# Optimization experiments

Measured on AMD Instinct MI355X. Metric: run time of the kernel, lower is better.

Reference implementation:

```python
import jax, jax.numpy as jnp
import numpy as np

N_NODES = 50000
N_EDGES = 800000
IN_FEATS = 128
HEADS = 4
OUT_FEATS = 32
NEG_SLOPE = 0.2


def setup_inputs() -> dict:
    key = jax.random.key(0)
    ks = jax.random.split(key, 9)
    HD = HEADS * OUT_FEATS
    return {
        "feat": jax.random.normal(ks[0], (N_NODES, IN_FEATS), dtype=jnp.float32),
        "W_src": jax.random.normal(ks[1], (HD, IN_FEATS), dtype=jnp.float32) * (1.0 / np.sqrt(IN_FEATS)),
        "b_src": jax.random.normal(ks[2], (HD,), dtype=jnp.float32) * 0.02,
        "W_dst": jax.random.normal(ks[3], (HD, IN_FEATS), dtype=jnp.float32) * (1.0 / np.sqrt(IN_FEATS)),
        "b_dst": jax.random.normal(ks[4], (HD,), dtype=jnp.float32) * 0.02,
        "W_v": jax.random.normal(ks[5], (HD, IN_FEATS), dtype=jnp.float32) * (1.0 / np.sqrt(IN_FEATS)),
        "b_v": jax.random.normal(ks[6], (HD,), dtype=jnp.float32) * 0.02,
        "src": jax.random.randint(ks[7], (N_EDGES,), 0, N_NODES, dtype=jnp.int32),
        "dst": jax.random.randint(ks[8], (N_EDGES,), 0, N_NODES, dtype=jnp.int32),
    }


def _edge_softmax(e, dst, n_nodes):
    # segment softmax over incoming edges of each dst node; e: [E, H, D]
    seg_max = jax.ops.segment_max(e, dst, num_segments=n_nodes)  # [N, H, D]
    ex = jnp.exp(e - seg_max[dst])
    seg_sum = jax.ops.segment_sum(ex, dst, num_segments=n_nodes)  # [N, H, D]
    return ex / seg_sum[dst]


def reference(feat, W_src, b_src, W_dst, b_dst, W_v, b_v, src, dst):
    n = feat.shape[0]
    # node projections -> [N, H, D]
    f_src = (feat @ W_src.T + b_src).reshape(n, HEADS, OUT_FEATS)
    f_dst = (feat @ W_dst.T + b_dst).reshape(n, HEADS, OUT_FEATS)
    f_v = (feat @ W_v.T + b_v).reshape(n, HEADS, OUT_FEATS)
    # per-edge additive attention (full feature vector, DGL u_add_v)
    a = f_src[src] + f_dst[dst]                       # [E, H, D]
    e = jnp.where(a >= 0, a, NEG_SLOPE * a)           # leaky_relu
    sa = _edge_softmax(e, dst, n)                     # [E, H, D]
    # weighted aggregate: u_mul_e then sum over incoming edges
    m = f_v[src] * sa                                 # [E, H, D]
    rst = jax.ops.segment_sum(m, dst, num_segments=n)  # [N, H, D]
    return rst.reshape(n, HEADS * OUT_FEATS)
```

## Files before the change

kernel.cpp:

```cpp
#include <hip/hip_runtime.h>
#include <hip/hip_fp16.h>

#define N_NODES 50000
#define N_EDGES 800000
#define IN_FEATS 128
#define HD 128
#define LOG2E 1.4426950408889634f

#define NB1 200
#define EPB1 4000
#define NBUK 196
#define MTAB (NBUK * NB1)
#define MB_SCAN 154
#define EBUF 6144

typedef __attribute__((ext_vector_type(8))) short bf16x8;
typedef __attribute__((ext_vector_type(4))) float floatx4;

#if __has_builtin(__builtin_amdgcn_exp2f)
#define EXP2F(x) __builtin_amdgcn_exp2f(x)
#else
#define EXP2F(x) __expf((x) * 0.6931471805599453f)
#endif

static __device__ __forceinline__ unsigned short f2bf(float x) {
    unsigned int u = __float_as_uint(x);
    return (unsigned short)((u + 0x7FFFu + ((u >> 16) & 1u)) >> 16);
}
static __device__ __forceinline__ float bf2f(unsigned short h) {
    return __uint_as_float((unsigned int)h << 16);
}
static __device__ __forceinline__ unsigned int pk(float a, float b) {
    return (unsigned int)__half_as_ushort(__float2half(a)) |
           ((unsigned int)__half_as_ushort(__float2half(b)) << 16);
}

__global__ __launch_bounds__(256) void prep_kernel(
    const float* __restrict__ W0, const float* __restrict__ W1,
    const float* __restrict__ W2, unsigned short* __restrict__ Bsw) {
    int idx = blockIdx.x * 256 + threadIdx.x;
    if (idx >= 24 * 4 * 64 * 8) return;
    int j = idx & 7;
    int l = (idx >> 3) & 63;
    int q = (idx >> 9) & 3;
    int t = idx >> 11;
    int k = q * 32 + ((l >> 4) << 3) + j;
    int c = ((t & 7) << 4) + (l & 15);
    int m = t >> 3;
    const float* W = (m == 0) ? W0 : ((m == 1) ? W1 : W2);
    float w = W[(size_t)c * IN_FEATS + k];
    if (m < 2) w *= LOG2E;
    Bsw[idx] = f2bf(w);
}

#define PGRID 782
__global__ __launch_bounds__(256) void proj_hist_kernel(
    const float* __restrict__ feat, const unsigned short* __restrict__ Bsw,
    const float* __restrict__ b_src, const float* __restrict__ b_dst,
    const float* __restrict__ b_v,
    unsigned short* __restrict__ gsv, unsigned short* __restrict__ fdh,
    const int* __restrict__ dst, int* __restrict__ Htab) {
    __shared__ int h[NBUK];
    if (blockIdx.x >= PGRID) {
        int blk = blockIdx.x - PGRID;
        for (int i = threadIdx.x; i < NBUK; i += 256) h[i] = 0;
        __syncthreads();
        int base = blk * EPB1;
        for (int i = threadIdx.x; i < EPB1; i += 256)
            atomicAdd(&h[dst[base + i] >> 8], 1);
        __syncthreads();
        for (int b = threadIdx.x; b < NBUK; b += 256)
            Htab[b * NB1 + blk] = h[b];
        return;
    }
    int wave = threadIdx.x >> 6, lane = threadIdx.x & 63;
    int tile = blockIdx.x * 4 + wave;
    if (tile >= N_NODES / 16) return;
    int row0 = tile * 16;
    int r16 = lane & 15, quad = lane >> 4;
    size_t node = (size_t)(row0 + r16);

    bf16x8 Fh[4], Fl[4];
    const float* frow = feat + node * IN_FEATS + quad * 8;
#pragma unroll
    for (int q = 0; q < 4; ++q) {
        float4 x0 = *(const float4*)(frow + q * 32);
        float4 x1 = *(const float4*)(frow + q * 32 + 4);
        float xs[8] = {x0.x, x0.y, x0.z, x0.w, x1.x, x1.y, x1.z, x1.w};
#pragma unroll
        for (int j = 0; j < 8; ++j) {
            unsigned short hh = f2bf(xs[j]);
            Fh[q][j] = (short)hh;
            Fl[q][j] = (short)f2bf(xs[j] - bf2f(hh));
        }
    }

#pragma unroll 1
    for (int tt = 0; tt < 8; ++tt) {
        floatx4 as = {0.f,0.f,0.f,0.f}, ad = {0.f,0.f,0.f,0.f}, av = {0.f,0.f,0.f,0.f};
#pragma unroll
        for (int q = 0; q < 4; ++q) {
            bf16x8 ws = *(const bf16x8*)(Bsw + ((((tt)      * 4 + q) * 64 + lane) << 3));
            bf16x8 wd = *(const bf16x8*)(Bsw + ((((8 + tt)  * 4 + q) * 64 + lane) << 3));
            bf16x8 wv = *(const bf16x8*)(Bsw + ((((16 + tt) * 4 + q) * 64 + lane) << 3));
            as = __builtin_amdgcn_mfma_f32_16x16x32_bf16(ws, Fh[q], as, 0, 0, 0);
            as = __builtin_amdgcn_mfma_f32_16x16x32_bf16(ws, Fl[q], as, 0, 0, 0);
            ad = __builtin_amdgcn_mfma_f32_16x16x32_bf16(wd, Fh[q], ad, 0, 0, 0);
            ad = __builtin_amdgcn_mfma_f32_16x16x32_bf16(wd, Fl[q], ad, 0, 0, 0);
            av = __builtin_amdgcn_mfma_f32_16x16x32_bf16(wv, Fh[q], av, 0, 0, 0);
            av = __builtin_amdgcn_mfma_f32_16x16x32_bf16(wv, Fl[q], av, 0, 0, 0);
        }
        int cbase = (tt << 4) + (quad << 2);
        float4 bs = *(const float4*)(b_src + cbase);
        float4 bd = *(const float4*)(b_dst + cbase);
        float4 bv = *(const float4*)(b_v   + cbase);
        uint4 o;
        o.x = pk(as[0] + bs.x * LOG2E, as[1] + bs.y * LOG2E);
        o.y = pk(av[0] + bv.x,         av[1] + bv.y);
        o.z = pk(as[2] + bs.z * LOG2E, as[3] + bs.w * LOG2E);
        o.w = pk(av[2] + bv.z,         av[3] + bv.w);
        *(uint4*)(gsv + node * 256 + (cbase << 1)) = o;
        uint2 od;
        od.x = pk(ad[0] + bd.x * LOG2E, ad[1] + bd.y * LOG2E);
        od.y = pk(ad[2] + bd.z * LOG2E, ad[3] + bd.w * LOG2E);
        *(uint2*)(fdh + node * 128 + cbase) = od;
    }
}

__global__ __launch_bounds__(256) void scan_partial(const int* __restrict__ cnt,
                                                    int* __restrict__ bsum, int n) {
    int i = blockIdx.x * 256 + threadIdx.x;
    int v = (i < n) ? cnt[i] : 0;
#pragma unroll
    for (int d = 32; d > 0; d >>= 1) v += __shfl_down(v, d);
    __shared__ int ws[4];
    int lane = threadIdx.x & 63, w = threadIdx.x >> 6;
    if (lane == 0) ws[w] = v;
    __syncthreads();
    if (threadIdx.x == 0) bsum[blockIdx.x] = ws[0] + ws[1] + ws[2] + ws[3];
}

__global__ __launch_bounds__(256) void scan_write2(const int* __restrict__ cnt,
                                                   const int* __restrict__ bsum,
                                                   int* __restrict__ outp, int n, int nb) {
    int t = threadIdx.x, b = blockIdx.x;
    int va = (t < nb) ? bsum[t] : 0;
    int vb = (t < b) ? va : 0;
    int ra = va, rb = vb;
#pragma unroll
    for (int d = 32; d > 0; d >>= 1) { ra += __shfl_down(ra, d); rb += __shfl_down(rb, d); }
    __shared__ int sa[4], sb[4], ws2[4];
    int lane = t & 63, w = t >> 6;
    if (lane == 0) { sa[w] = ra; sb[w] = rb; }
    __syncthreads();
    int total = sa[0] + sa[1] + sa[2] + sa[3];
    int base  = sb[0] + sb[1] + sb[2] + sb[3];
    int i = b * 256 + t;
    int v = (i < n) ? cnt[i] : 0;
    int x = v;
#pragma unroll
    for (int d = 1; d < 64; d <<= 1) { int up = __shfl_up(x, d); if (lane >= d) x += up; }
    if (lane == 63) ws2[w] = x;
    __syncthreads();
    for (int ww = 0; ww < w; ++ww) base += ws2[ww];
    if (i < n) outp[i] = base + x - v;
    if (b == (int)gridDim.x - 1 && t == 0) outp[n] = total;
}

__global__ __launch_bounds__(256) void scatter1_kernel(
    const int* __restrict__ src, const int* __restrict__ dst,
    const int* __restrict__ HtabS, unsigned int* __restrict__ tmp) {
    __shared__ int cur[NBUK];
    int blk = blockIdx.x;
    for (int b = threadIdx.x; b < NBUK; b += 256) cur[b] = HtabS[b * NB1 + blk];
    __syncthreads();
    int base = blk * EPB1;
    for (int i = threadIdx.x; i < EPB1; i += 256) {
        int d = dst[base + i];
        int s = src[base + i];
        int p = atomicAdd(&cur[d >> 8], 1);
        tmp[p] = (unsigned int)s | ((unsigned int)(d & 255) << 16);
    }
}

__global__ __launch_bounds__(256) void bin_kernel(
    const unsigned int* __restrict__ tmp, const int* __restrict__ HtabS,
    int* __restrict__ off, int* __restrict__ ssort) {
    __shared__ unsigned int ebuf[EBUF];
    __shared__ int cnt_l[256];
    __shared__ int wsum[4];
    int b = blockIdx.x, t = threadIdx.x;
    int start = HtabS[b * NB1];
    int end = (b == NBUK - 1) ? N_EDGES : HtabS[(b + 1) * NB1];
    int cnt0 = end - start;
    cnt_l[t] = 0;
    __syncthreads();
    bool staged = (cnt0 <= EBUF);
    for (int i = t; i < cnt0; i += 256) {
        unsigned int e = tmp[start + i];
        if (staged) ebuf[i] = e;
        atomicAdd(&cnt_l[e >> 16], 1);
    }
    __syncthreads();
    int v = cnt_l[t];
    int lane = t & 63, w = t >> 6;
    int x = v;
#pragma unroll
    for (int d = 1; d < 64; d <<= 1) { int up = __shfl_up(x, d); if (lane >= d) x += up; }
    if (lane == 63) wsum[w] = x;
    __syncthreads();
    int basex = 0;
    for (int ww = 0; ww < w; ++ww) basex += wsum[ww];
    int excl = basex + x - v;
    int node = b * 256 + t;
    if (node < N_NODES) off[node] = start + excl;
    if (b == NBUK - 1 && t == 0) { off[N_NODES] = N_EDGES; ssort[N_EDGES] = 0; }
    __syncthreads();
    cnt_l[t] = excl;
    __syncthreads();
    for (int i = t; i < cnt0; i += 256) {
        unsigned int e = staged ? ebuf[i] : tmp[start + i];
        int p = atomicAdd(&cnt_l[e >> 16], 1);
        ssort[start + p] = (int)(e & 0xFFFFu);
    }
}

__global__ __launch_bounds__(256) void gather_kernel(
    const unsigned short* __restrict__ gsv, const unsigned short* __restrict__ fdh,
    const int* __restrict__ off, const int* __restrict__ ssort,
    float* __restrict__ out, int n) {
    int wid = __builtin_amdgcn_readfirstlane((int)((blockIdx.x * 256 + threadIdx.x) >> 6));
    int lane = threadIdx.x & 63;
    if (wid >= n) return;
    float2 fd = __half22float2(*(const __half2*)(fdh + (size_t)wid * 128 + lane * 2));

    float nxA = 0.f, nyA = 0.f, dxA = 0.f, dyA = 0.f;
    float nxB = 0.f, nyB = 0.f, dxB = 0.f, dyB = 0.f;
    int beg = off[wid], end = off[wid + 1];
    int mid = (beg + end) >> 1;
    int LA = mid - beg, LB = end - mid;

#define EDGE_UPD(g, valid, dxv, dyv, nxv, nyv) {                              \
        float2 fs = __half22float2(*(const __half2*)&(g).x);                  \
        float a0 = fs.x + fd.x, a1 = fs.y + fd.y;                             \
        a0 = fmaf(fminf(a0, 0.f), -0.8f, a0);                                 \
        a1 = fmaf(fminf(a1, 0.f), -0.8f, a1);                                 \
        float x0 = EXP2F(a0), x1 = EXP2F(a1);                                 \
        if (!(valid)) { x0 = 0.f; x1 = 0.f; }                                 \
        float2 fv = __half22float2(*(const __half2*)&(g).y);                  \
        dxv += x0; dyv += x1;                                                 \
        nxv = fmaf(x0, fv.x, nxv); nyv = fmaf(x1, fv.y, nyv); }

    if (LB > 0) {
        int sA = ssort[beg];
        int sB = ssort[mid];
        uint2 gA = *(const uint2*)(gsv + (size_t)sA * 256 + lane * 4);
        uint2 gB = *(const uint2*)(gsv + (size_t)sB * 256 + lane * 4);
        for (int k = 0; k < LB - 1; ++k) {
            int sA2 = ssort[beg + k + 1];
            int sB2 = ssort[mid + k + 1];
            uint2 gA2 = *(const uint2*)(gsv + (size_t)sA2 * 256 + lane * 4);
            uint2 gB2 = *(const uint2*)(gsv + (size_t)sB2 * 256 + lane * 4);
            EDGE_UPD(gA, 1, dxA, dyA, nxA, nyA);
            EDGE_UPD(gB, 1, dxB, dyB, nxB, nyB);
            gA = gA2; gB = gB2;
        }
        EDGE_UPD(gA, (LB - 1) < LA, dxA, dyA, nxA, nyA);
        EDGE_UPD(gB, 1, dxB, dyB, nxB, nyB);
    }
    float dx = dxA + dxB, dy = dyA + dyB;
    float nx = nxA + nxB, ny = nyA + nyB;
    float2 o;
    o.x = (dx > 0.f) ? nx / dx : 0.f;
    o.y = (dy > 0.f) ? ny / dy : 0.f;
    *(float2*)&out[(size_t)wid * HD + lane * 2] = o;
#undef EDGE_UPD
}

extern "C" void kernel_launch(void* const* d_in, const int* in_sizes, int n_in,
                              void* d_out, int out_size, void* d_ws, size_t ws_size,
                              hipStream_t stream) {
    const float* feat  = (const float*)d_in[0];
    const float* W_src = (const float*)d_in[1];
    const float* b_src = (const float*)d_in[2];
    const float* W_dst = (const float*)d_in[3];
    const float* b_dst = (const float*)d_in[4];
    const float* W_v   = (const float*)d_in[5];
    const float* b_v   = (const float*)d_in[6];
    const int*   src   = (const int*)d_in[7];
    const int*   dst   = (const int*)d_in[8];
    float* out = (float*)d_out;

    unsigned short* gsv = (unsigned short*)d_ws;
    unsigned short* fdh = gsv + (size_t)N_NODES * 256;
    unsigned short* Bsw = fdh + (size_t)N_NODES * 128;
    int* Htab  = (int*)(Bsw + 24 * 4 * 64 * 8);
    int* HtabS = Htab + MTAB;
    int* bsum  = HtabS + MTAB + 1;
    int* off   = bsum + 256;
    int* ssort = off + (N_NODES + 1);
    unsigned int* tmp = (unsigned int*)(ssort + N_EDGES + 1);

    prep_kernel<<<192, 256, 0, stream>>>(W_src, W_dst, W_v, Bsw);

    proj_hist_kernel<<<PGRID + NB1, 256, 0, stream>>>(
        feat, Bsw, b_src, b_dst, b_v, gsv, fdh, dst, Htab);

    scan_partial<<<MB_SCAN, 256, 0, stream>>>(Htab, bsum, MTAB);
    scan_write2<<<MB_SCAN, 256, 0, stream>>>(Htab, bsum, HtabS, MTAB, MB_SCAN);

    scatter1_kernel<<<NB1, 256, 0, stream>>>(src, dst, HtabS, tmp);
    bin_kernel<<<NBUK, 256, 0, stream>>>(tmp, HtabS, off, ssort);

    gather_kernel<<<(N_NODES * 64) / 256, 256, 0, stream>>>(gsv, fdh, off, ssort, out, N_NODES);
}
```

Baseline: 196.1 us.

## Fuse histogram into prep, scan+scatter into projection, cut launches

Moves the per-block dst histogram into the weight-prep launch and stores counts as 16-bit values. The projection launch now also runs the scatter: each scatter block redundantly scans the whole histogram table to find its own offsets. The separate scan kernels and scatter kernel are removed, bin_kernel derives its bucket range by reduction, and staged bins write ssort coalesced through a shared buffer. Gather now uses 128-thread blocks. Launch count and global scan traffic drop, at the cost of redundant per-block scanning of a 39k-entry table.

```diff
diff --git a/kernel.cpp b/kernel.cpp
--- a/kernel.cpp
+++ b/kernel.cpp
@@ -11,8 +11,9 @@
 #define EPB1 4000
 #define NBUK 196
 #define MTAB (NBUK * NB1)
-#define MB_SCAN 154
 #define EBUF 6144
+#define PREPN 192
+#define PGRID 782
 
 typedef __attribute__((ext_vector_type(8))) short bf16x8;
 typedef __attribute__((ext_vector_type(4))) float floatx4;
@@ -35,42 +36,84 @@
            ((unsigned int)__half_as_ushort(__float2half(b)) << 16);
 }
 
-__global__ __launch_bounds__(256) void prep_kernel(
+__global__ __launch_bounds__(256) void prep_hist_kernel(
     const float* __restrict__ W0, const float* __restrict__ W1,
-    const float* __restrict__ W2, unsigned short* __restrict__ Bsw) {
-    int idx = blockIdx.x * 256 + threadIdx.x;
-    if (idx >= 24 * 4 * 64 * 8) return;
-    int j = idx & 7;
-    int l = (idx >> 3) & 63;
-    int q = (idx >> 9) & 3;
-    int t = idx >> 11;
-    int k = q * 32 + ((l >> 4) << 3) + j;
-    int c = ((t & 7) << 4) + (l & 15);
-    int m = t >> 3;
-    const float* W = (m == 0) ? W0 : ((m == 1) ? W1 : W2);
-    float w = W[(size_t)c * IN_FEATS + k];
-    if (m < 2) w *= LOG2E;
-    Bsw[idx] = f2bf(w);
-}
-
-#define PGRID 782
-__global__ __launch_bounds__(256) void proj_hist_kernel(
+    const float* __restrict__ W2, unsigned short* __restrict__ Bsw,
+    const int* __restrict__ dst, unsigned short* __restrict__ Htab) {
+    __shared__ int h[NBUK];
+    if (blockIdx.x < PREPN) {
+        int idx = blockIdx.x * 256 + threadIdx.x;
+        int j = idx & 7;
+        int l = (idx >> 3) & 63;
+        int q = (idx >> 9) & 3;
+        int t = idx >> 11;
+        int k = q * 32 + ((l >> 4) << 3) + j;
+        int c = ((t & 7) << 4) + (l & 15);
+        int m = t >> 3;
+        const float* W = (m == 0) ? W0 : ((m == 1) ? W1 : W2);
+        float w = W[(size_t)c * IN_FEATS + k];
+        if (m < 2) w *= LOG2E;
+        Bsw[idx] = f2bf(w);
+        return;
+    }
+    int blk = blockIdx.x - PREPN;
+    for (int i = threadIdx.x; i < NBUK; i += 256) h[i] = 0;
+    __syncthreads();
+    int base = blk * EPB1;
+    for (int i = threadIdx.x; i < EPB1; i += 256)
+        atomicAdd(&h[dst[base + i] >> 8], 1);
+    __syncthreads();
+    for (int b = threadIdx.x; b < NBUK; b += 256)
+        Htab[b * NB1 + blk] = (unsigned short)h[b];
+}
+
+__global__ __launch_bounds__(256) void proj_scatter_kernel(
     const float* __restrict__ feat, const unsigned short* __restrict__ Bsw,
     const float* __restrict__ b_src, const float* __restrict__ b_dst,
     const float* __restrict__ b_v,
     unsigned short* __restrict__ gsv, unsigned short* __restrict__ fdh,
-    const int* __restrict__ dst, int* __restrict__ Htab) {
-    __shared__ int h[NBUK];
+    const int* __restrict__ src, const int* __restrict__ dst,
+    const unsigned short* __restrict__ Htab, unsigned int* __restrict__ tmp) {
+    __shared__ int Sl[NBUK];
+    __shared__ int curl[NBUK];
+    __shared__ int wsums[4];
+    __shared__ int sbase;
     if (blockIdx.x >= PGRID) {
         int blk = blockIdx.x - PGRID;
-        for (int i = threadIdx.x; i < NBUK; i += 256) h[i] = 0;
+        int t = threadIdx.x, lane = t & 63, w = t >> 6;
+        if (t == 0) sbase = 0;
         __syncthreads();
-        int base = blk * EPB1;
-        for (int i = threadIdx.x; i < EPB1; i += 256)
-            atomicAdd(&h[dst[base + i] >> 8], 1);
+        for (int T = 0; T < MTAB; T += 256) {
+            int f = T + t;
+            int v = (f < MTAB) ? (int)Htab[f] : 0;
+            int x = v;
+#pragma unroll
+            for (int d = 1; d < 64; d <<= 1) {
+                int up = __shfl_up(x, d);
+                if (lane >= d) x += up;
+            }
+            if (lane == 63) wsums[w] = x;
+            __syncthreads();
+            int base = sbase;
+            for (int ww = 0; ww < w; ++ww) base += wsums[ww];
+            int tile_total = wsums[0] + wsums[1] + wsums[2] + wsums[3];
+            if (f < MTAB) {
+                int bq = f / NB1;
+                if (f - bq * NB1 == blk) Sl[bq] = base + x - v;
+            }
+            __syncthreads();
+            if (t == 0) sbase += tile_total;
+        }
         __syncthreads();
-        for (int b = threadIdx.x; b < NBUK; b += 256)
-            Htab[b * NB1 + blk] = h[b];
+        for (int bb = t; bb < NBUK; bb += 256) curl[bb] = Sl[bb];
+        __syncthreads();
+        int ebase = blk * EPB1;
+        for (int i = t; i < EPB1; i += 256) {
+            int d = dst[ebase + i];
+            int s = src[ebase + i];
+            int p = atomicAdd(&curl[d >> 8], 1);
+            tmp[p] = (unsigned int)s | ((unsigned int)(d & 255) << 16);
+        }
         return;
     }
     int wave = threadIdx.x >> 6, lane = threadIdx.x & 63;
@@ -127,74 +170,36 @@
     }
 }
 
-__global__ __launch_bounds__(256) void scan_partial(const int* __restrict__ cnt,
-                                                    int* __restrict__ bsum, int n) {
-    int i = blockIdx.x * 256 + threadIdx.x;
-    int v = (i < n) ? cnt[i] : 0;
-#pragma unroll
-    for (int d = 32; d > 0; d >>= 1) v += __shfl_down(v, d);
-    __shared__ int ws[4];
-    int lane = threadIdx.x & 63, w = threadIdx.x >> 6;
-    if (lane == 0) ws[w] = v;
-    __syncthreads();
-    if (threadIdx.x == 0) bsum[blockIdx.x] = ws[0] + ws[1] + ws[2] + ws[3];
-}
-
-__global__ __launch_bounds__(256) void scan_write2(const int* __restrict__ cnt,
-                                                   const int* __restrict__ bsum,
-                                                   int* __restrict__ outp, int n, int nb) {
-    int t = threadIdx.x, b = blockIdx.x;
-    int va = (t < nb) ? bsum[t] : 0;
-    int vb = (t < b) ? va : 0;
-    int ra = va, rb = vb;
-#pragma unroll
-    for (int d = 32; d > 0; d >>= 1) { ra += __shfl_down(ra, d); rb += __shfl_down(rb, d); }
-    __shared__ int sa[4], sb[4], ws2[4];
-    int lane = t & 63, w = t >> 6;
-    if (lane == 0) { sa[w] = ra; sb[w] = rb; }
-    __syncthreads();
-    int total = sa[0] + sa[1] + sa[2] + sa[3];
-    int base  = sb[0] + sb[1] + sb[2] + sb[3];
-    int i = b * 256 + t;
-    int v = (i < n) ? cnt[i] : 0;
-    int x = v;
-#pragma unroll
-    for (int d = 1; d < 64; d <<= 1) { int up = __shfl_up(x, d); if (lane >= d) x += up; }
-    if (lane == 63) ws2[w] = x;
-    __syncthreads();
-    for (int ww = 0; ww < w; ++ww) base += ws2[ww];
-    if (i < n) outp[i] = base + x - v;
-    if (b == (int)gridDim.x - 1 && t == 0) outp[n] = total;
-}
-
-__global__ __launch_bounds__(256) void scatter1_kernel(
-    const int* __restrict__ src, const int* __restrict__ dst,
-    const int* __restrict__ HtabS, unsigned int* __restrict__ tmp) {
-    __shared__ int cur[NBUK];
-    int blk = blockIdx.x;
-    for (int b = threadIdx.x; b < NBUK; b += 256) cur[b] = HtabS[b * NB1 + blk];
-    __syncthreads();
-    int base = blk * EPB1;
-    for (int i = threadIdx.x; i < EPB1; i += 256) {
-        int d = dst[base + i];
-        int s = src[base + i];
-        int p = atomicAdd(&cur[d >> 8], 1);
-        tmp[p] = (unsigned int)s | ((unsigned int)(d & 255) << 16);
-    }
-}
-
 __global__ __launch_bounds__(256) void bin_kernel(
-    const unsigned int* __restrict__ tmp, const int* __restrict__ HtabS,
+    const unsigned int* __restrict__ tmp, const unsigned short* __restrict__ Htab,
     int* __restrict__ off, int* __restrict__ ssort) {
     __shared__ unsigned int ebuf[EBUF];
+    __shared__ unsigned short obuf[EBUF];
     __shared__ int cnt_l[256];
     __shared__ int wsum[4];
-    int b = blockIdx.x, t = threadIdx.x;
-    int start = HtabS[b * NB1];
-    int end = (b == NBUK - 1) ? N_EDGES : HtabS[(b + 1) * NB1];
-    int cnt0 = end - start;
+    __shared__ int sred[8];
+    int b = blockIdx.x, t = threadIdx.x, lane = t & 63, w = t >> 6;
+
+    int lo = b * NB1, hi = lo + NB1;
+    int sAll = 0, sBuk = 0;
+    for (int f = t; f < hi; f += 256) {
+        int v = (int)Htab[f];
+        sAll += v;
+        sBuk += (f >= lo) ? v : 0;
+    }
+#pragma unroll
+    for (int d = 32; d > 0; d >>= 1) {
+        sAll += __shfl_down(sAll, d);
+        sBuk += __shfl_down(sBuk, d);
+    }
+    if (lane == 0) { sred[w] = sAll; sred[4 + w] = sBuk; }
     cnt_l[t] = 0;
     __syncthreads();
+    int end  = sred[0] + sred[1] + sred[2] + sred[3];
+    int btot = sred[4] + sred[5] + sred[6] + sred[7];
+    int start = end - btot;
+    int cnt0 = btot;
+
     bool staged = (cnt0 <= EBUF);
     for (int i = t; i < cnt0; i += 256) {
         unsigned int e = tmp[start + i];
@@ -203,7 +208,6 @@
     }
     __syncthreads();
     int v = cnt_l[t];
-    int lane = t & 63, w = t >> 6;
     int x = v;
 #pragma unroll
     for (int d = 1; d < 64; d <<= 1) { int up = __shfl_up(x, d); if (lane >= d) x += up; }
@@ -218,18 +222,29 @@
     __syncthreads();
     cnt_l[t] = excl;
     __syncthreads();
-    for (int i = t; i < cnt0; i += 256) {
-        unsigned int e = staged ? ebuf[i] : tmp[start + i];
-        int p = atomicAdd(&cnt_l[e >> 16], 1);
-        ssort[start + p] = (int)(e & 0xFFFFu);
-    }
-}
-
-__global__ __launch_bounds__(256) void gather_kernel(
+    if (staged) {
+        for (int i = t; i < cnt0; i += 256) {
+            unsigned int e = ebuf[i];
+            int p = atomicAdd(&cnt_l[e >> 16], 1);
+            obuf[p] = (unsigned short)(e & 0xFFFFu);
+        }
+        __syncthreads();
+        for (int i = t; i < cnt0; i += 256)
+            ssort[start + i] = (int)obuf[i];
+    } else {
+        for (int i = t; i < cnt0; i += 256) {
+            unsigned int e = tmp[start + i];
+            int p = atomicAdd(&cnt_l[e >> 16], 1);
+            ssort[start + p] = (int)(e & 0xFFFFu);
+        }
+    }
+}
+
+__global__ __launch_bounds__(128) void gather_kernel(
     const unsigned short* __restrict__ gsv, const unsigned short* __restrict__ fdh,
     const int* __restrict__ off, const int* __restrict__ ssort,
     float* __restrict__ out, int n) {
-    int wid = __builtin_amdgcn_readfirstlane((int)((blockIdx.x * 256 + threadIdx.x) >> 6));
+    int wid = __builtin_amdgcn_readfirstlane((int)((blockIdx.x * 128 + threadIdx.x) >> 6));
     int lane = threadIdx.x & 63;
     if (wid >= n) return;
     float2 fd = __half22float2(*(const __half2*)(fdh + (size_t)wid * 128 + lane * 2));
@@ -291,26 +306,20 @@
     const int*   dst   = (const int*)d_in[8];
     float* out = (float*)d_out;
 
-    unsigned short* gsv = (unsigned short*)d_ws;
-    unsigned short* fdh = gsv + (size_t)N_NODES * 256;
-    unsigned short* Bsw = fdh + (size_t)N_NODES * 128;
-    int* Htab  = (int*)(Bsw + 24 * 4 * 64 * 8);
-    int* HtabS = Htab + MTAB;
-    int* bsum  = HtabS + MTAB + 1;
-    int* off   = bsum + 256;
+    unsigned short* gsv  = (unsigned short*)d_ws;
+    unsigned short* fdh  = gsv + (size_t)N_NODES * 256;
+    unsigned short* Bsw  = fdh + (size_t)N_NODES * 128;
+    unsigned short* Htab = Bsw + 24 * 4 * 64 * 8;
+    int* off   = (int*)(Htab + MTAB + (MTAB & 1));
     int* ssort = off + (N_NODES + 1);
     unsigned int* tmp = (unsigned int*)(ssort + N_EDGES + 1);
 
-    prep_kernel<<<192, 256, 0, stream>>>(W_src, W_dst, W_v, Bsw);
-
-    proj_hist_kernel<<<PGRID + NB1, 256, 0, stream>>>(
-        feat, Bsw, b_src, b_dst, b_v, gsv, fdh, dst, Htab);
-
-    scan_partial<<<MB_SCAN, 256, 0, stream>>>(Htab, bsum, MTAB);
-    scan_write2<<<MB_SCAN, 256, 0, stream>>>(Htab, bsum, HtabS, MTAB, MB_SCAN);
-
-    scatter1_kernel<<<NB1, 256, 0, stream>>>(src, dst, HtabS, tmp);
-    bin_kernel<<<NBUK, 256, 0, stream>>>(tmp, HtabS, off, ssort);
-
-    gather_kernel<<<(N_NODES * 64) / 256, 256, 0, stream>>>(gsv, fdh, off, ssort, out, N_NODES);
-}
+    prep_hist_kernel<<<PREPN + NB1, 256, 0, stream>>>(W_src, W_dst, W_v, Bsw, dst, Htab);
+
+    proj_scatter_kernel<<<PGRID + NB1, 256, 0, stream>>>(
+        feat, Bsw, b_src, b_dst, b_v, gsv, fdh, src, dst, Htab, tmp);
+
+    bin_kernel<<<NBUK, 256, 0, stream>>>(tmp, Htab, off, ssort);
+
+    gather_kernel<<<(N_NODES * 64) / 128, 128, 0, stream>>>(gsv, fdh, off, ssort, out, N_NODES);
+}
```

Result: slower. 292.2 us (+49.0%).

## Regroup stages to overlap projection with scatter and widen gather per-lane loads

Applied to the files above, without the earlier changes.

The weight prep now runs in the same launch as the dst histogram, and the node projection shares a launch with the edge scatter. This removes one kernel launch and lets the projection overlap the scatter work. The histogram table is stored as 16-bit counts. bin_kernel stages sorted sources in LDS so the writes to ssort are coalesced. The gather kernel splits each wave into two halves that handle alternating edges with 16-byte loads, then merges them with a cross-half shuffle, using 128-thread blocks.

```diff
diff --git a/kernel.cpp b/kernel.cpp
--- a/kernel.cpp
+++ b/kernel.cpp
@@ -13,6 +13,8 @@
 #define MTAB (NBUK * NB1)
 #define MB_SCAN 154
 #define EBUF 6144
+#define PREPN 192
+#define PGRID 782
 
 typedef __attribute__((ext_vector_type(8))) short bf16x8;
 typedef __attribute__((ext_vector_type(4))) float floatx4;
@@ -35,42 +37,96 @@
            ((unsigned int)__half_as_ushort(__float2half(b)) << 16);
 }
 
-__global__ __launch_bounds__(256) void prep_kernel(
+__global__ __launch_bounds__(256) void prep_hist_kernel(
     const float* __restrict__ W0, const float* __restrict__ W1,
-    const float* __restrict__ W2, unsigned short* __restrict__ Bsw) {
-    int idx = blockIdx.x * 256 + threadIdx.x;
-    if (idx >= 24 * 4 * 64 * 8) return;
-    int j = idx & 7;
-    int l = (idx >> 3) & 63;
-    int q = (idx >> 9) & 3;
-    int t = idx >> 11;
-    int k = q * 32 + ((l >> 4) << 3) + j;
-    int c = ((t & 7) << 4) + (l & 15);
-    int m = t >> 3;
-    const float* W = (m == 0) ? W0 : ((m == 1) ? W1 : W2);
-    float w = W[(size_t)c * IN_FEATS + k];
-    if (m < 2) w *= LOG2E;
-    Bsw[idx] = f2bf(w);
-}
-
-#define PGRID 782
-__global__ __launch_bounds__(256) void proj_hist_kernel(
+    const float* __restrict__ W2, unsigned short* __restrict__ Bsw,
+    const int* __restrict__ dst, unsigned short* __restrict__ Htab) {
+    __shared__ int h[NBUK];
+    if (blockIdx.x < PREPN) {
+        int idx = blockIdx.x * 256 + threadIdx.x;
+        int j = idx & 7;
+        int l = (idx >> 3) & 63;
+        int q = (idx >> 9) & 3;
+        int t = idx >> 11;
+        int k = q * 32 + ((l >> 4) << 3) + j;
+        int c = ((t & 7) << 4) + (l & 15);
+        int m = t >> 3;
+        const float* W = (m == 0) ? W0 : ((m == 1) ? W1 : W2);
+        float w = W[(size_t)c * IN_FEATS + k];
+        if (m < 2) w *= LOG2E;
+        Bsw[idx] = f2bf(w);
+        return;
+    }
+    int blk = blockIdx.x - PREPN;
+    for (int i = threadIdx.x; i < NBUK; i += 256) h[i] = 0;
+    __syncthreads();
+    int base = blk * EPB1;
+    for (int i = threadIdx.x; i < EPB1; i += 256)
+        atomicAdd(&h[dst[base + i] >> 8], 1);
+    __syncthreads();
+    for (int b = threadIdx.x; b < NBUK; b += 256)
+        Htab[b * NB1 + blk] = (unsigned short)h[b];
+}
+
+__global__ __launch_bounds__(256) void scan_partial(const unsigned short* __restrict__ cnt,
+                                                    int* __restrict__ bsum, int n) {
+    int i = blockIdx.x * 256 + threadIdx.x;
+    int v = (i < n) ? (int)cnt[i] : 0;
+#pragma unroll
+    for (int d = 32; d > 0; d >>= 1) v += __shfl_down(v, d);
+    __shared__ int ws[4];
+    int lane = threadIdx.x & 63, w = threadIdx.x >> 6;
+    if (lane == 0) ws[w] = v;
+    __syncthreads();
+    if (threadIdx.x == 0) bsum[blockIdx.x] = ws[0] + ws[1] + ws[2] + ws[3];
+}
+
+__global__ __launch_bounds__(256) void scan_write2(const unsigned short* __restrict__ cnt,
+                                                   const int* __restrict__ bsum,
+                                                   int* __restrict__ outp, int n, int nb) {
+    int t = threadIdx.x, b = blockIdx.x;
+    int va = (t < nb) ? bsum[t] : 0;
+    int vb = (t < b) ? va : 0;
+    int ra = va, rb = vb;
+#pragma unroll
+    for (int d = 32; d > 0; d >>= 1) { ra += __shfl_down(ra, d); rb += __shfl_down(rb, d); }
+    __shared__ int sa[4], sb[4], ws2[4];
+    int lane = t & 63, w = t >> 6;
+    if (lane == 0) { sa[w] = ra; sb[w] = rb; }
+    __syncthreads();
+    int total = sa[0] + sa[1] + sa[2] + sa[3];
+    int base  = sb[0] + sb[1] + sb[2] + sb[3];
+    int i = b * 256 + t;
+    int v = (i < n) ? (int)cnt[i] : 0;
+    int x = v;
+#pragma unroll
+    for (int d = 1; d < 64; d <<= 1) { int up = __shfl_up(x, d); if (lane >= d) x += up; }
+    if (lane == 63) ws2[w] = x;
+    __syncthreads();
+    for (int ww = 0; ww < w; ++ww) base += ws2[ww];
+    if (i < n) outp[i] = base + x - v;
+    if (b == (int)gridDim.x - 1 && t == 0) outp[n] = total;
+}
+
+__global__ __launch_bounds__(256) void proj_scatter_kernel(
     const float* __restrict__ feat, const unsigned short* __restrict__ Bsw,
     const float* __restrict__ b_src, const float* __restrict__ b_dst,
     const float* __restrict__ b_v,
     unsigned short* __restrict__ gsv, unsigned short* __restrict__ fdh,
-    const int* __restrict__ dst, int* __restrict__ Htab) {
-    __shared__ int h[NBUK];
+    const int* __restrict__ src, const int* __restrict__ dst,
+    const int* __restrict__ HtabS, unsigned int* __restrict__ tmp) {
+    __shared__ int curl[NBUK];
     if (blockIdx.x >= PGRID) {
         int blk = blockIdx.x - PGRID;
-        for (int i = threadIdx.x; i < NBUK; i += 256) h[i] = 0;
+        for (int b = threadIdx.x; b < NBUK; b += 256) curl[b] = HtabS[b * NB1 + blk];
         __syncthreads();
-        int base = blk * EPB1;
-        for (int i = threadIdx.x; i < EPB1; i += 256)
-            atomicAdd(&h[dst[base + i] >> 8], 1);
-        __syncthreads();
-        for (int b = threadIdx.x; b < NBUK; b += 256)
-            Htab[b * NB1 + blk] = h[b];
+        int ebase = blk * EPB1;
+        for (int i = threadIdx.x; i < EPB1; i += 256) {
+            int d = dst[ebase + i];
+            int s = src[ebase + i];
+            int p = atomicAdd(&curl[d >> 8], 1);
+            tmp[p] = (unsigned int)s | ((unsigned int)(d & 255) << 16);
+        }
         return;
     }
     int wave = threadIdx.x >> 6, lane = threadIdx.x & 63;
@@ -127,69 +183,14 @@
     }
 }
 
-__global__ __launch_bounds__(256) void scan_partial(const int* __restrict__ cnt,
-                                                    int* __restrict__ bsum, int n) {
-    int i = blockIdx.x * 256 + threadIdx.x;
-    int v = (i < n) ? cnt[i] : 0;
-#pragma unroll
-    for (int d = 32; d > 0; d >>= 1) v += __shfl_down(v, d);
-    __shared__ int ws[4];
-    int lane = threadIdx.x & 63, w = threadIdx.x >> 6;
-    if (lane == 0) ws[w] = v;
-    __syncthreads();
-    if (threadIdx.x == 0) bsum[blockIdx.x] = ws[0] + ws[1] + ws[2] + ws[3];
-}
-
-__global__ __launch_bounds__(256) void scan_write2(const int* __restrict__ cnt,
-                                                   const int* __restrict__ bsum,
-                                                   int* __restrict__ outp, int n, int nb) {
-    int t = threadIdx.x, b = blockIdx.x;
-    int va = (t < nb) ? bsum[t] : 0;
-    int vb = (t < b) ? va : 0;
-    int ra = va, rb = vb;
-#pragma unroll
-    for (int d = 32; d > 0; d >>= 1) { ra += __shfl_down(ra, d); rb += __shfl_down(rb, d); }
-    __shared__ int sa[4], sb[4], ws2[4];
-    int lane = t & 63, w = t >> 6;
-    if (lane == 0) { sa[w] = ra; sb[w] = rb; }
-    __syncthreads();
-    int total = sa[0] + sa[1] + sa[2] + sa[3];
-    int base  = sb[0] + sb[1] + sb[2] + sb[3];
-    int i = b * 256 + t;
-    int v = (i < n) ? cnt[i] : 0;
-    int x = v;
-#pragma unroll
-    for (int d = 1; d < 64; d <<= 1) { int up = __shfl_up(x, d); if (lane >= d) x += up; }
-    if (lane == 63) ws2[w] = x;
-    __syncthreads();
-    for (int ww = 0; ww < w; ++ww) base += ws2[ww];
-    if (i < n) outp[i] = base + x - v;
-    if (b == (int)gridDim.x - 1 && t == 0) outp[n] = total;
-}
-
-__global__ __launch_bounds__(256) void scatter1_kernel(
-    const int* __restrict__ src, const int* __restrict__ dst,
-    const int* __restrict__ HtabS, unsigned int* __restrict__ tmp) {
-    __shared__ int cur[NBUK];
-    int blk = blockIdx.x;
-    for (int b = threadIdx.x; b < NBUK; b += 256) cur[b] = HtabS[b * NB1 + blk];
-    __syncthreads();
-    int base = blk * EPB1;
-    for (int i = threadIdx.x; i < EPB1; i += 256) {
-        int d = dst[base + i];
-        int s = src[base + i];
-        int p = atomicAdd(&cur[d >> 8], 1);
-        tmp[p] = (unsigned int)s | ((unsigned int)(d & 255) << 16);
-    }
-}
-
 __global__ __launch_bounds__(256) void bin_kernel(
     const unsigned int* __restrict__ tmp, const int* __restrict__ HtabS,
     int* __restrict__ off, int* __restrict__ ssort) {
     __shared__ unsigned int ebuf[EBUF];
+    __shared__ unsigned short obuf[EBUF];
     __shared__ int cnt_l[256];
     __shared__ int wsum[4];
-    int b = blockIdx.x, t = threadIdx.x;
+    int b = blockIdx.x, t = threadIdx.x, lane = t & 63, w = t >> 6;
     int start = HtabS[b * NB1];
     int end = (b == NBUK - 1) ? N_EDGES : HtabS[(b + 1) * NB1];
     int cnt0 = end - start;
@@ -203,7 +204,6 @@
     }
     __syncthreads();
     int v = cnt_l[t];
-    int lane = t & 63, w = t >> 6;
     int x = v;
 #pragma unroll
     for (int d = 1; d < 64; d <<= 1) { int up = __shfl_up(x, d); if (lane >= d) x += up; }
@@ -214,67 +214,90 @@
     int excl = basex + x - v;
     int node = b * 256 + t;
     if (node < N_NODES) off[node] = start + excl;
-    if (b == NBUK - 1 && t == 0) { off[N_NODES] = N_EDGES; ssort[N_EDGES] = 0; }
+    if (b == NBUK - 1) {
+        if (t == 0) off[N_NODES] = N_EDGES;
+        if (t < 4) ssort[N_EDGES + t] = 0;
+    }
     __syncthreads();
     cnt_l[t] = excl;
     __syncthreads();
-    for (int i = t; i < cnt0; i += 256) {
-        unsigned int e = staged ? ebuf[i] : tmp[start + i];
-        int p = atomicAdd(&cnt_l[e >> 16], 1);
-        ssort[start + p] = (int)(e & 0xFFFFu);
-    }
-}
-
-__global__ __launch_bounds__(256) void gather_kernel(
+    if (staged) {
+        for (int i = t; i < cnt0; i += 256) {
+            unsigned int e = ebuf[i];
+            int p = atomicAdd(&cnt_l[e >> 16], 1);
+            obuf[p] = (unsigned short)(e & 0xFFFFu);
+        }
+        __syncthreads();
+        for (int i = t; i < cnt0; i += 256)
+            ssort[start + i] = (int)obuf[i];
+    } else {
+        for (int i = t; i < cnt0; i += 256) {
+            unsigned int e = tmp[start + i];
+            int p = atomicAdd(&cnt_l[e >> 16], 1);
+            ssort[start + p] = (int)(e & 0xFFFFu);
+        }
+    }
+}
+
+__global__ __launch_bounds__(128) void gather_kernel(
     const unsigned short* __restrict__ gsv, const unsigned short* __restrict__ fdh,
     const int* __restrict__ off, const int* __restrict__ ssort,
     float* __restrict__ out, int n) {
-    int wid = __builtin_amdgcn_readfirstlane((int)((blockIdx.x * 256 + threadIdx.x) >> 6));
+    int wid = __builtin_amdgcn_readfirstlane((int)((blockIdx.x * 128 + threadIdx.x) >> 6));
     int lane = threadIdx.x & 63;
     if (wid >= n) return;
-    float2 fd = __half22float2(*(const __half2*)(fdh + (size_t)wid * 128 + lane * 2));
-
-    float nxA = 0.f, nyA = 0.f, dxA = 0.f, dyA = 0.f;
-    float nxB = 0.f, nyB = 0.f, dxB = 0.f, dyB = 0.f;
+    int half = lane >> 5;
+    int grp = lane & 31;
+    uint2 fdraw = *(const uint2*)(fdh + (size_t)wid * 128 + grp * 4);
+    float2 fd01 = __half22float2(*(const __half2*)&fdraw.x);
+    float2 fd23 = __half22float2(*(const __half2*)&fdraw.y);
+
+    float n0=0.f,n1=0.f,n2=0.f,n3=0.f,d0=0.f,d1=0.f,d2=0.f,d3=0.f;
     int beg = off[wid], end = off[wid + 1];
-    int mid = (beg + end) >> 1;
-    int LA = mid - beg, LB = end - mid;
-
-#define EDGE_UPD(g, valid, dxv, dyv, nxv, nyv) {                              \
-        float2 fs = __half22float2(*(const __half2*)&(g).x);                  \
-        float a0 = fs.x + fd.x, a1 = fs.y + fd.y;                             \
-        a0 = fmaf(fminf(a0, 0.f), -0.8f, a0);                                 \
-        a1 = fmaf(fminf(a1, 0.f), -0.8f, a1);                                 \
-        float x0 = EXP2F(a0), x1 = EXP2F(a1);                                 \
-        if (!(valid)) { x0 = 0.f; x1 = 0.f; }                                 \
-        float2 fv = __half22float2(*(const __half2*)&(g).y);                  \
-        dxv += x0; dyv += x1;                                                 \
-        nxv = fmaf(x0, fv.x, nxv); nyv = fmaf(x1, fv.y, nyv); }
-
-    if (LB > 0) {
-        int sA = ssort[beg];
-        int sB = ssort[mid];
-        uint2 gA = *(const uint2*)(gsv + (size_t)sA * 256 + lane * 4);
-        uint2 gB = *(const uint2*)(gsv + (size_t)sB * 256 + lane * 4);
-        for (int k = 0; k < LB - 1; ++k) {
-            int sA2 = ssort[beg + k + 1];
-            int sB2 = ssort[mid + k + 1];
-            uint2 gA2 = *(const uint2*)(gsv + (size_t)sA2 * 256 + lane * 4);
-            uint2 gB2 = *(const uint2*)(gsv + (size_t)sB2 * 256 + lane * 4);
-            EDGE_UPD(gA, 1, dxA, dyA, nxA, nyA);
-            EDGE_UPD(gB, 1, dxB, dyB, nxB, nyB);
-            gA = gA2; gB = gB2;
-        }
-        EDGE_UPD(gA, (LB - 1) < LA, dxA, dyA, nxA, nyA);
-        EDGE_UPD(gB, 1, dxB, dyB, nxB, nyB);
-    }
-    float dx = dxA + dxB, dy = dyA + dyB;
-    float nx = nxA + nxB, ny = nyA + nyB;
-    float2 o;
-    o.x = (dx > 0.f) ? nx / dx : 0.f;
-    o.y = (dy > 0.f) ? ny / dy : 0.f;
-    *(float2*)&out[(size_t)wid * HD + lane * 2] = o;
-#undef EDGE_UPD
+    int deg = end - beg;
+    int iters = (deg + 1) >> 1;
+
+#define EDGE_UPD4(g, valid) {                                                  \
+    float2 fs01 = __half22float2(*(const __half2*)&(g).x);                     \
+    float2 fv01 = __half22float2(*(const __half2*)&(g).y);                     \
+    float2 fs23 = __half22float2(*(const __half2*)&(g).z);                     \
+    float2 fv23 = __half22float2(*(const __half2*)&(g).w);                     \
+    float a0 = fs01.x + fd01.x, a1 = fs01.y + fd01.y;                          \
+    float a2 = fs23.x + fd23.x, a3 = fs23.y + fd23.y;                          \
+    a0 = fmaf(fminf(a0, 0.f), -0.8f, a0);                                      \
+    a1 = fmaf(fminf(a1, 0.f), -0.8f, a1);                                      \
+    a2 = fmaf(fminf(a2, 0.f), -0.8f, a2);                                      \
+    a3 = fmaf(fminf(a3, 0.f), -0.8f, a3);                                      \
+    float x0 = EXP2F(a0), x1 = EXP2F(a1), x2 = EXP2F(a2), x3 = EXP2F(a3);      \
+    if (!(valid)) { x0 = 0.f; x1 = 0.f; x2 = 0.f; x3 = 0.f; }                  \
+    d0 += x0; d1 += x1; d2 += x2; d3 += x3;                                    \
+    n0 = fmaf(x0, fv01.x, n0); n1 = fmaf(x1, fv01.y, n1);                      \
+    n2 = fmaf(x2, fv23.x, n2); n3 = fmaf(x3, fv23.y, n3); }
+
+    if (iters > 0) {
+        int s = ssort[beg + half];
+        uint4 g = *(const uint4*)(gsv + (size_t)s * 256 + grp * 8);
+        for (int k = 0; k < iters - 1; ++k) {
+            int s2 = ssort[beg + 2 * k + 2 + half];
+            uint4 g2 = *(const uint4*)(gsv + (size_t)s2 * 256 + grp * 8);
+            EDGE_UPD4(g, 1);
+            g = g2;
+        }
+        EDGE_UPD4(g, (half == 0) | ((deg & 1) == 0));
+    }
+    d0 += __shfl_xor(d0, 32); d1 += __shfl_xor(d1, 32);
+    d2 += __shfl_xor(d2, 32); d3 += __shfl_xor(d3, 32);
+    n0 += __shfl_xor(n0, 32); n1 += __shfl_xor(n1, 32);
+    n2 += __shfl_xor(n2, 32); n3 += __shfl_xor(n3, 32);
+    if (half == 0) {
+        float4 o;
+        o.x = (d0 > 0.f) ? n0 / d0 : 0.f;
+        o.y = (d1 > 0.f) ? n1 / d1 : 0.f;
+        o.z = (d2 > 0.f) ? n2 / d2 : 0.f;
+        o.w = (d3 > 0.f) ? n3 / d3 : 0.f;
+        *(float4*)&out[(size_t)wid * HD + grp * 4] = o;
+    }
+#undef EDGE_UPD4
 }
 
 extern "C" void kernel_launch(void* const* d_in, const int* in_sizes, int n_in,
@@ -291,26 +314,25 @@
     const int*   dst   = (const int*)d_in[8];
     float* out = (float*)d_out;
 
-    unsigned short* gsv = (unsigned short*)d_ws;
-    unsigned short* fdh = gsv + (size_t)N_NODES * 256;
-    unsigned short* Bsw = fdh + (size_t)N_NODES * 128;
-    int* Htab  = (int*)(Bsw + 24 * 4 * 64 * 8);
-    int* HtabS = Htab + MTAB;
+    unsigned short* gsv  = (unsigned short*)d_ws;
+    unsigned short* fdh  = gsv + (size_t)N_NODES * 256;
+    unsigned short* Bsw  = fdh + (size_t)N_NODES * 128;
+    unsigned short* Htab = Bsw + 24 * 4 * 64 * 8;
+    int* HtabS = (int*)(Htab + MTAB);
     int* bsum  = HtabS + MTAB + 1;
     int* off   = bsum + 256;
     int* ssort = off + (N_NODES + 1);
-    unsigned int* tmp = (unsigned int*)(ssort + N_EDGES + 1);
-
-    prep_kernel<<<192, 256, 0, stream>>>(W_src, W_dst, W_v, Bsw);
-
-    proj_hist_kernel<<<PGRID + NB1, 256, 0, stream>>>(
-        feat, Bsw, b_src, b_dst, b_v, gsv, fdh, dst, Htab);
+    unsigned int* tmp = (unsigned int*)(ssort + N_EDGES + 4);
+
+    prep_hist_kernel<<<PREPN + NB1, 256, 0, stream>>>(W_src, W_dst, W_v, Bsw, dst, Htab);
 
     scan_partial<<<MB_SCAN, 256, 0, stream>>>(Htab, bsum, MTAB);
     scan_write2<<<MB_SCAN, 256, 0, stream>>>(Htab, bsum, HtabS, MTAB, MB_SCAN);
 
-    scatter1_kernel<<<NB1, 256, 0, stream>>>(src, dst, HtabS, tmp);
+    proj_scatter_kernel<<<PGRID + NB1, 256, 0, stream>>>(
+        feat, Bsw, b_src, b_dst, b_v, gsv, fdh, src, dst, HtabS, tmp);
+
     bin_kernel<<<NBUK, 256, 0, stream>>>(tmp, HtabS, off, ssort);
 
-    gather_kernel<<<(N_NODES * 64) / 256, 256, 0, stream>>>(gsv, fdh, off, ssort, out, N_NODES);
-}
+    gather_kernel<<<(N_NODES * 64) / 128, 128, 0, stream>>>(gsv, fdh, off, ssort, out, N_NODES);
+}
```

New measurement: 190.8 us. 2.7% less time.
